# Optimization experiments

Hardware: AMD Instinct MI355X
Metric: run time of the kernel (lower is better)

Reference implementation:

```python
import jax, jax.numpy as jnp
import numpy as np

P, OBS, H, MSG, EMB, A = 2048, 512, 2048, 16, 32, 3
SLOPE = 0.01  # LeakyReLU default negative slope


def setup_inputs() -> dict:
    key = jax.random.key(0)
    ks = jax.random.split(key, 12)
    s = 0.02
    return {
        "obs": jax.random.normal(ks[0], (P, OBS), jnp.float32),
        "messages": jnp.zeros((P, MSG), jnp.float32),
        "embeddings": jnp.zeros((P, EMB), jnp.float32),
        "h": jnp.zeros((1, H), jnp.float32),
        "w_ih": jax.random.normal(ks[1], (3 * H, OBS), jnp.float32) * s,
        "w_hh": jax.random.normal(ks[2], (3 * H, H), jnp.float32) * s,
        "b_ih": jax.random.normal(ks[3], (3 * H,), jnp.float32) * s,
        "b_hh": jax.random.normal(ks[4], (3 * H,), jnp.float32) * s,
        "ff_w": jax.random.normal(ks[5], (2, H), jnp.float32) * s,
        "ff_b": jnp.zeros((2,), jnp.float32),
        "ap_w": jax.random.normal(ks[6], (A, H), jnp.float32) * s,
        "ap_b": jnp.zeros((A,), jnp.float32),
        "dp_w": jax.random.normal(ks[7], (A, H), jnp.float32) * s,
        "dp_b": jnp.zeros((A,), jnp.float32),
        "v_w": jax.random.normal(ks[8], (1, H), jnp.float32) * s,
        "v_b": jnp.zeros((1,), jnp.float32),
    }


def reference(obs, messages, embeddings, h, w_ih, w_hh, b_ih, b_hh,
              ff_w, ff_b, ap_w, ap_b, dp_w, dp_b, v_w, v_b):
    # h arg is ignored (module re-initializes it to zeros).
    hid = w_hh.shape[1]
    # precompute input-side GRU gates for all players: [P, 3H]
    gi_all = obs @ w_ih.T + b_ih

    def step(hc, gi):  # hc: [H]
        gh = hc @ w_hh.T + b_hh
        ir, iz, inn = jnp.split(gi, 3)
        hr, hz, hn = jnp.split(gh, 3)
        r = jax.nn.sigmoid(ir + hr)
        z = jax.nn.sigmoid(iz + hz)
        n = jnp.tanh(inn + r * hn)
        h_new = (1.0 - z) * n + z * hc
        return h_new, h_new

    h0 = jnp.zeros((hid,), obs.dtype)
    _, hs = jax.lax.scan(step, h0, gi_all)  # [P, H]

    acts = hs @ ff_w.T + ff_b                      # [P, 2]
    acts = jnp.where(acts >= 0, acts, SLOPE * acts)  # LeakyReLU
    a_w = jax.nn.softmax(acts[:, 0])               # softmax over players
    d_w = jax.nn.softmax(acts[:, 1])
    a_att = a_w @ hs                               # [H]
    d_att = d_w @ hs
    a_pol = a_att @ ap_w.T + ap_b
    d_pol = d_att @ dp_w.T + dp_b
    v = (a_att + d_att) @ v_w.T + v_b
    return (a_pol, d_pol, v)
```

## Files before the change

### kernel.cpp

```cpp
#include <hip/hip_runtime.h>
#include <cstdint>
#include <cstddef>

#define P_N  2048
#define OBS_N 512
#define H_N  2048
#define G3H  6144

__device__ __forceinline__ float wave_sum(float v) {
#pragma unroll
  for (int off = 32; off > 0; off >>= 1) v += __shfl_xor(v, off);
  return v;
}
__device__ __forceinline__ float wave_max(float v) {
#pragma unroll
  for (int off = 32; off > 0; off >>= 1) v = fmaxf(v, __shfl_xor(v, off));
  return v;
}

__global__ __launch_bounds__(256, 2) void gi_gemm(
    const float* __restrict__ A,
    const float* __restrict__ B,
    const float* __restrict__ bias,
    float* __restrict__ C)
{
  constexpr int BM = 128, BK = 32, LDP = BM + 4;
  __shared__ float As[BK][LDP];
  __shared__ float Bs[BK][LDP];
  const int tid = threadIdx.x;
  const int bm = blockIdx.y * BM;
  const int bn = blockIdx.x * BM;
  const int tx = tid & 15, ty = tid >> 4;
  const int lrow = tid >> 3;
  const int lk4  = (tid & 7) << 2;

  float acc[8][8];
#pragma unroll
  for (int i = 0; i < 8; ++i)
#pragma unroll
    for (int j = 0; j < 8; ++j) acc[i][j] = 0.f;

  for (int k0 = 0; k0 < OBS_N; k0 += BK) {
#pragma unroll
    for (int i = 0; i < 4; ++i) {
      const int r = lrow + 32 * i;
      float4 av = *(const float4*)(A + (size_t)(bm + r) * OBS_N + k0 + lk4);
      float4 bv = *(const float4*)(B + (size_t)(bn + r) * OBS_N + k0 + lk4);
      As[lk4 + 0][r] = av.x; As[lk4 + 1][r] = av.y;
      As[lk4 + 2][r] = av.z; As[lk4 + 3][r] = av.w;
      Bs[lk4 + 0][r] = bv.x; Bs[lk4 + 1][r] = bv.y;
      Bs[lk4 + 2][r] = bv.z; Bs[lk4 + 3][r] = bv.w;
    }
    __syncthreads();
#pragma unroll
    for (int k = 0; k < BK; ++k) {
      float4 a0 = *(const float4*)&As[k][ty * 4];
      float4 a1 = *(const float4*)&As[k][64 + ty * 4];
      float4 b0 = *(const float4*)&Bs[k][tx * 4];
      float4 b1 = *(const float4*)&Bs[k][64 + tx * 4];
      float a[8] = {a0.x, a0.y, a0.z, a0.w, a1.x, a1.y, a1.z, a1.w};
      float b[8] = {b0.x, b0.y, b0.z, b0.w, b1.x, b1.y, b1.z, b1.w};
#pragma unroll
      for (int i = 0; i < 8; ++i)
#pragma unroll
        for (int j = 0; j < 8; ++j)
          acc[i][j] = fmaf(a[i], b[j], acc[i][j]);
    }
    __syncthreads();
  }

  float4 bs0 = *(const float4*)(bias + bn + tx * 4);
  float4 bs1 = *(const float4*)(bias + bn + 64 + tx * 4);
  const float bb[8] = {bs0.x, bs0.y, bs0.z, bs0.w, bs1.x, bs1.y, bs1.z, bs1.w};
#pragma unroll
  for (int i = 0; i < 8; ++i) {
    const int row = bm + ((i < 4) ? (ty * 4 + i) : (64 + ty * 4 + i - 4));
    float4 o0 = {acc[i][0] + bb[0], acc[i][1] + bb[1], acc[i][2] + bb[2], acc[i][3] + bb[3]};
    float4 o1 = {acc[i][4] + bb[4], acc[i][5] + bb[5], acc[i][6] + bb[6], acc[i][7] + bb[7]};
    *(float4*)(C + (size_t)row * G3H + bn + tx * 4) = o0;
    *(float4*)(C + (size_t)row * G3H + bn + 64 + tx * 4) = o1;
  }
}

#define AGW(reg, val) \
  asm volatile("v_accvgpr_write_b32 " reg ", %0" :: "v"(val) : reg)
#define AGR(reg, dst) \
  asm volatile("v_accvgpr_read_b32 %0, " reg : "=v"(dst) :: reg)

#define LOADK_(koff, r0a,r0b,r0c,r0d, r1a,r1b,r1c,r1d, r2a,r2b,r2c,r2d) do { \
    float4 A_ = *(const float4*)(p0 + (koff) * 256 + l4); \
    float4 B_ = *(const float4*)(p1 + (koff) * 256 + l4); \
    float4 C_ = *(const float4*)(p2 + (koff) * 256 + l4); \
    AGW(r0a, A_.x); AGW(r0b, A_.y); AGW(r0c, A_.z); AGW(r0d, A_.w); \
    AGW(r1a, B_.x); AGW(r1b, B_.y); AGW(r1c, B_.z); AGW(r1d, B_.w); \
    AGW(r2a, C_.x); AGW(r2b, C_.y); AGW(r2c, C_.z); AGW(r2d, C_.w); \
  } while (0)

#define GEMVK_(koff, r0a,r0b,r0c,r0d, r1a,r1b,r1c,r1d, r2a,r2b,r2c,r2d) do { \
    float4 hv = *(const float4*)&hbuf[(koff) * 256 + l4]; \
    float tw; \
    AGR(r0a, tw); acc0 = fmaf(tw, hv.x, acc0); \
    AGR(r0b, tw); acc0 = fmaf(tw, hv.y, acc0); \
    AGR(r0c, tw); acc0 = fmaf(tw, hv.z, acc0); \
    AGR(r0d, tw); acc0 = fmaf(tw, hv.w, acc0); \
    AGR(r1a, tw); acc1 = fmaf(tw, hv.x, acc1); \
    AGR(r1b, tw); acc1 = fmaf(tw, hv.y, acc1); \
    AGR(r1c, tw); acc1 = fmaf(tw, hv.z, acc1); \
    AGR(r1d, tw); acc1 = fmaf(tw, hv.w, acc1); \
    AGR(r2a, tw); acc2 = fmaf(tw, hv.x, acc2); \
    AGR(r2b, tw); acc2 = fmaf(tw, hv.y, acc2); \
    AGR(r2c, tw); acc2 = fmaf(tw, hv.z, acc2); \
    AGR(r2d, tw); acc2 = fmaf(tw, hv.w, acc2); \
  } while (0)

#define LOADK(...) LOADK_(__VA_ARGS__)
#define GEMVK(...) GEMVK_(__VA_ARGS__)

#define KL0 "a0","a1","a2","a3",    "a32","a33","a34","a35", "a64","a65","a66","a67"
#define KL1 "a4","a5","a6","a7",    "a36","a37","a38","a39", "a68","a69","a70","a71"
#define KL2 "a8","a9","a10","a11",  "a40","a41","a42","a43", "a72","a73","a74","a75"
#define KL3 "a12","a13","a14","a15","a44","a45","a46","a47", "a76","a77","a78","a79"
#define KL4 "a16","a17","a18","a19","a48","a49","a50","a51", "a80","a81","a82","a83"
#define KL5 "a20","a21","a22","a23","a52","a53","a54","a55", "a84","a85","a86","a87"
#define KL6 "a24","a25","a26","a27","a56","a57","a58","a59", "a88","a89","a90","a91"
#define KL7 "a28","a29","a30","a31","a60","a61","a62","a63", "a92","a93","a94","a95"

__global__ __launch_bounds__(512, 1) void gru_scan(
    const float* __restrict__ w_hh,
    const float* __restrict__ b_hh,
    const float* __restrict__ gi,
    float* __restrict__ hs,
    unsigned long long* mb)
{
  __shared__ __align__(16) float hbuf[H_N];
  const int g   = blockIdx.x;
  const int tid = threadIdx.x;
  const int w   = tid >> 6;
  const int l   = tid & 63;
  const int l4  = l * 4;
  const int j   = (g << 3) + w;

  {
    const float* p0 = w_hh + (size_t)j * H_N;
    const float* p1 = w_hh + (size_t)(H_N + j) * H_N;
    const float* p2 = w_hh + (size_t)(2 * H_N + j) * H_N;
    LOADK(0, KL0); LOADK(1, KL1); LOADK(2, KL2); LOADK(3, KL3);
    LOADK(4, KL4); LOADK(5, KL5); LOADK(6, KL6); LOADK(7, KL7);
  }
  const float bh0 = b_hh[j], bh1 = b_hh[H_N + j], bh2 = b_hh[2 * H_N + j];
  float hprev = 0.f;

  for (int t = 0; t < P_N; ++t) {
    const float ir  = gi[(size_t)t * G3H + j];
    const float iz  = gi[(size_t)t * G3H + H_N + j];
    const float inn = gi[(size_t)t * G3H + 2 * H_N + j];

    float acc0 = 0.f, acc1 = 0.f, acc2 = 0.f;
    if (t > 0) {
      unsigned long long* src = mb + (size_t)((t - 1) & 1) * H_N + tid * 4;
      float h0 = 0.f, h1 = 0.f, h2 = 0.f, h3 = 0.f;
      unsigned pend = 0xFu;
      const unsigned tag = (unsigned)t;
      while (pend) {
#pragma unroll
        for (int q = 0; q < 4; ++q) {
          if (pend & (1u << q)) {
            unsigned long long v =
                __hip_atomic_load(src + q, __ATOMIC_RELAXED, __HIP_MEMORY_SCOPE_AGENT);
            if ((unsigned)(v >> 32) == tag) {
              float f = __uint_as_float((unsigned)(v & 0xffffffffull));
              if (q == 0) h0 = f; else if (q == 1) h1 = f;
              else if (q == 2) h2 = f; else h3 = f;
              pend &= ~(1u << q);
            }
          }
        }
        if (pend) __builtin_amdgcn_s_sleep(1);
      }
      __syncthreads();
      *(float4*)&hbuf[tid * 4] = make_float4(h0, h1, h2, h3);
      __syncthreads();

      GEMVK(0, KL0); GEMVK(1, KL1); GEMVK(2, KL2); GEMVK(3, KL3);
      GEMVK(4, KL4); GEMVK(5, KL5); GEMVK(6, KL6); GEMVK(7, KL7);

#pragma unroll
      for (int off = 32; off > 0; off >>= 1) {
        acc0 += __shfl_xor(acc0, off);
        acc1 += __shfl_xor(acc1, off);
        acc2 += __shfl_xor(acc2, off);
      }
    }

    const float r = 1.f / (1.f + __expf(-(ir + acc0 + bh0)));
    const float z = 1.f / (1.f + __expf(-(iz + acc1 + bh1)));
    const float narg = inn + r * (acc2 + bh2);
    const float e2 = __expf(2.f * narg);
    const float n = (e2 - 1.f) / (e2 + 1.f);
    const float hnew = (1.f - z) * n + z * hprev;
    hprev = hnew;

    if (l == 0) {
      hs[(size_t)t * H_N + j] = hnew;
      unsigned long long pk = ((unsigned long long)(unsigned)(t + 1) << 32) |
                              (unsigned long long)__float_as_uint(hnew);
      __hip_atomic_store(mb + (size_t)(t & 1) * H_N + j, pk,
                         __ATOMIC_RELAXED, __HIP_MEMORY_SCOPE_AGENT);
    }
  }
}

__global__ __launch_bounds__(512) void acts_kernel(
    const float* __restrict__ hs, const float* __restrict__ ff_w,
    const float* __restrict__ ff_b, float* __restrict__ acts)
{
  const int w = threadIdx.x >> 6, l = threadIdx.x & 63;
  const int p = blockIdx.x * 8 + w;
  const float* hrow = hs + (size_t)p * H_N;
  float sa = 0.f, sd = 0.f;
#pragma unroll
  for (int k = 0; k < 8; ++k) {
    float4 hv = *(const float4*)(hrow + k * 256 + l * 4);
    float4 fa = *(const float4*)(ff_w + k * 256 + l * 4);
    float4 fd = *(const float4*)(ff_w + H_N + k * 256 + l * 4);
    sa += hv.x * fa.x + hv.y * fa.y + hv.z * fa.z + hv.w * fa.w;
    sd += hv.x * fd.x + hv.y * fd.y + hv.z * fd.z + hv.w * fd.w;
  }
  sa = wave_sum(sa); sd = wave_sum(sd);
  if (l == 0) {
    float a = sa + ff_b[0];
    float d = sd + ff_b[1];
    a = (a >= 0.f) ? a : 0.01f * a;
    d = (d >= 0.f) ? d : 0.01f * d;
    acts[p] = a;
    acts[P_N + p] = d;
  }
}

__global__ __launch_bounds__(256) void softmax_kernel(
    const float* __restrict__ acts, float* __restrict__ wts)
{
  __shared__ float red[4];
  __shared__ float bcast;
  const int tid = threadIdx.x;
  const int w = tid >> 6, l = tid & 63;
  for (int c = 0; c < 2; ++c) {
    const float* x = acts + c * P_N;
    float* y = wts + c * P_N;
    float m = -3.4e38f;
    for (int i = tid; i < P_N; i += 256) m = fmaxf(m, x[i]);
    m = wave_max(m);
    if (l == 0) red[w] = m;
    __syncthreads();
    if (tid == 0) bcast = fmaxf(fmaxf(red[0], red[1]), fmaxf(red[2], red[3]));
    __syncthreads();
    const float M = bcast;
    float s = 0.f;
    for (int i = tid; i < P_N; i += 256) {
      float e = __expf(x[i] - M);
      y[i] = e;
      s += e;
    }
    s = wave_sum(s);
    __syncthreads();
    if (l == 0) red[w] = s;
    __syncthreads();
    if (tid == 0) bcast = 1.f / (red[0] + red[1] + red[2] + red[3]);
    __syncthreads();
    const float inv = bcast;
    for (int i = tid; i < P_N; i += 256) y[i] *= inv;
    __syncthreads();
  }
}

__global__ __launch_bounds__(256) void pool_kernel(
    const float* __restrict__ hs, const float* __restrict__ wts,
    float* __restrict__ att)
{
  const int g = blockIdx.x;
  const int tid = threadIdx.x;
  const int c0 = tid * 8;
  float aa[8] = {0, 0, 0, 0, 0, 0, 0, 0};
  float dd[8] = {0, 0, 0, 0, 0, 0, 0, 0};
  for (int r = 0; r < 16; ++r) {
    const int p = g * 16 + r;
    const float wa = wts[p];
    const float wd = wts[P_N + p];
    const float* hp = hs + (size_t)p * H_N + c0;
    float4 h0 = *(const float4*)hp;
    float4 h1 = *(const float4*)(hp + 4);
    aa[0] = fmaf(wa, h0.x, aa[0]); aa[1] = fmaf(wa, h0.y, aa[1]);
    aa[2] = fmaf(wa, h0.z, aa[2]); aa[3] = fmaf(wa, h0.w, aa[3]);
    aa[4] = fmaf(wa, h1.x, aa[4]); aa[5] = fmaf(wa, h1.y, aa[5]);
    aa[6] = fmaf(wa, h1.z, aa[6]); aa[7] = fmaf(wa, h1.w, aa[7]);
    dd[0] = fmaf(wd, h0.x, dd[0]); dd[1] = fmaf(wd, h0.y, dd[1]);
    dd[2] = fmaf(wd, h0.z, dd[2]); dd[3] = fmaf(wd, h0.w, dd[3]);
    dd[4] = fmaf(wd, h1.x, dd[4]); dd[5] = fmaf(wd, h1.y, dd[5]);
    dd[6] = fmaf(wd, h1.z, dd[6]); dd[7] = fmaf(wd, h1.w, dd[7]);
  }
#pragma unroll
  for (int q = 0; q < 8; ++q) {
    atomicAdd(&att[c0 + q], aa[q]);
    atomicAdd(&att[H_N + c0 + q], dd[q]);
  }
}

__global__ __launch_bounds__(512) void head_kernel(
    const float* __restrict__ att,
    const float* __restrict__ ap_w, const float* __restrict__ ap_b,
    const float* __restrict__ dp_w, const float* __restrict__ dp_b,
    const float* __restrict__ v_w, const float* __restrict__ v_b,
    float* __restrict__ out)
{
  const int w = threadIdx.x >> 6, l = threadIdx.x & 63;
  if (w >= 7) return;
  float s = 0.f;
  if (w < 3) {
    const float* m = ap_w + (size_t)w * H_N;
    for (int k = 0; k < 32; ++k) { int i = k * 64 + l; s += att[i] * m[i]; }
  } else if (w < 6) {
    const float* m = dp_w + (size_t)(w - 3) * H_N;
    for (int k = 0; k < 32; ++k) { int i = k * 64 + l; s += att[H_N + i] * m[i]; }
  } else {
    for (int k = 0; k < 32; ++k) { int i = k * 64 + l; s += (att[i] + att[H_N + i]) * v_w[i]; }
  }
  s = wave_sum(s);
  if (l == 0) {
    float b = (w < 3) ? ap_b[w] : ((w < 6) ? dp_b[w - 3] : v_b[0]);
    out[w] = s + b;
  }
}

extern "C" void kernel_launch(void* const* d_in, const int* in_sizes, int n_in,
                              void* d_out, int out_size, void* d_ws, size_t ws_size,
                              hipStream_t stream) {
  const float* obs  = (const float*)d_in[0];
  const float* w_ih = (const float*)d_in[4];
  const float* w_hh = (const float*)d_in[5];
  const float* b_ih = (const float*)d_in[6];
  const float* b_hh = (const float*)d_in[7];
  const float* ff_w = (const float*)d_in[8];
  const float* ff_b = (const float*)d_in[9];
  const float* ap_w = (const float*)d_in[10];
  const float* ap_b = (const float*)d_in[11];
  const float* dp_w = (const float*)d_in[12];
  const float* dp_b = (const float*)d_in[13];
  const float* v_w  = (const float*)d_in[14];
  const float* v_b  = (const float*)d_in[15];
  float* out = (float*)d_out;

  float* gi = (float*)d_ws;
  float* hs = gi + (size_t)P_N * G3H;
  unsigned long long* mb = (unsigned long long*)(hs + (size_t)P_N * H_N);
  float* acts = (float*)(mb + 2 * H_N);
  float* wts  = acts + 2 * P_N;
  float* att  = wts + 2 * P_N;

  hipMemsetAsync(mb, 0, 2 * H_N * sizeof(unsigned long long), stream);
  hipMemsetAsync(att, 0, 2 * H_N * sizeof(float), stream);

  gi_gemm<<<dim3(G3H / 128, P_N / 128), 256, 0, stream>>>(obs, w_ih, b_ih, gi);
  gru_scan<<<256, 512, 0, stream>>>(w_hh, b_hh, gi, hs, mb);
  acts_kernel<<<P_N / 8, 512, 0, stream>>>(hs, ff_w, ff_b, acts);
  softmax_kernel<<<1, 256, 0, stream>>>(acts, wts);
  pool_kernel<<<128, 256, 0, stream>>>(hs, wts, att);
  head_kernel<<<1, 512, 0, stream>>>(att, ap_w, ap_b, dp_w, dp_b, v_w, v_b, out);
}
```

Measured before the change: 10.89 ms.

## Add per-block step flags to GRU scan and write hs rows coalesced

Adds a per-block flag array that each workgroup bumps after finishing a step. Wave 0 polls all 256 flags before the other waves read the tagged hidden values, so most of the polling moves onto one wave. It also drops the scattered per-lane hs stores and has one rotating block write each full hs row from shared memory. The cost is an extra barrier and flag store per step, plus a second polling phase that may add latency on the critical path.

Measured after the change: 8.769 ms. 1.24x faster.

```diff
diff --git a/kernel.cpp b/kernel.cpp
--- a/kernel.cpp
+++ b/kernel.cpp
@@ -130,7 +130,8 @@
     const float* __restrict__ b_hh,
     const float* __restrict__ gi,
     float* __restrict__ hs,
-    unsigned long long* mb)
+    unsigned long long* mb,
+    unsigned* flags)
 {
   __shared__ __align__(16) float hbuf[H_N];
   const int g   = blockIdx.x;
@@ -157,10 +158,28 @@
 
     float acc0 = 0.f, acc1 = 0.f, acc2 = 0.f;
     if (t > 0) {
-      unsigned long long* src = mb + (size_t)((t - 1) & 1) * H_N + tid * 4;
+      const unsigned tag = (unsigned)t;
+      const int par = (t - 1) & 1;
+
+      if (w == 0) {
+        const unsigned long long exp2 =
+            (unsigned long long)tag * 0x100000001ULL;
+        unsigned long long* fp =
+            (unsigned long long*)(flags + (size_t)par * 256) + 2 * l;
+        for (;;) {
+          unsigned long long f0 =
+              __hip_atomic_load(fp + 0, __ATOMIC_RELAXED, __HIP_MEMORY_SCOPE_AGENT);
+          unsigned long long f1 =
+              __hip_atomic_load(fp + 1, __ATOMIC_RELAXED, __HIP_MEMORY_SCOPE_AGENT);
+          if (__all(f0 == exp2 && f1 == exp2)) break;
+          __builtin_amdgcn_s_sleep(1);
+        }
+      }
+      __syncthreads();
+
+      unsigned long long* src = mb + (size_t)par * H_N + tid * 4;
       float h0 = 0.f, h1 = 0.f, h2 = 0.f, h3 = 0.f;
       unsigned pend = 0xFu;
-      const unsigned tag = (unsigned)t;
       while (pend) {
 #pragma unroll
         for (int q = 0; q < 4; ++q) {
@@ -177,9 +196,13 @@
         }
         if (pend) __builtin_amdgcn_s_sleep(1);
       }
-      __syncthreads();
       *(float4*)&hbuf[tid * 4] = make_float4(h0, h1, h2, h3);
       __syncthreads();
+
+      if (g == ((t - 1) & 255)) {
+        *(float4*)(hs + (size_t)(t - 1) * H_N + tid * 4) =
+            *(const float4*)&hbuf[tid * 4];
+      }
 
       GEMVK(0, KL0); GEMVK(1, KL1); GEMVK(2, KL2); GEMVK(3, KL3);
       GEMVK(4, KL4); GEMVK(5, KL5); GEMVK(6, KL6); GEMVK(7, KL7);
@@ -201,13 +224,19 @@
     hprev = hnew;
 
     if (l == 0) {
-      hs[(size_t)t * H_N + j] = hnew;
       unsigned long long pk = ((unsigned long long)(unsigned)(t + 1) << 32) |
                               (unsigned long long)__float_as_uint(hnew);
       __hip_atomic_store(mb + (size_t)(t & 1) * H_N + j, pk,
                          __ATOMIC_RELAXED, __HIP_MEMORY_SCOPE_AGENT);
     }
-  }
+    __syncthreads();
+    if (tid == 0) {
+      __hip_atomic_store(flags + (size_t)(t & 1) * 256 + g, (unsigned)(t + 1),
+                         __ATOMIC_RELAXED, __HIP_MEMORY_SCOPE_AGENT);
+    }
+  }
+
+  if (l == 0) hs[(size_t)(P_N - 1) * H_N + j] = hprev;
 }
 
 __global__ __launch_bounds__(512) void acts_kernel(
@@ -352,15 +381,16 @@
   float* gi = (float*)d_ws;
   float* hs = gi + (size_t)P_N * G3H;
   unsigned long long* mb = (unsigned long long*)(hs + (size_t)P_N * H_N);
-  float* acts = (float*)(mb + 2 * H_N);
+  unsigned* flags = (unsigned*)(mb + 2 * H_N);
+  float* acts = (float*)(flags + 2 * 256);
   float* wts  = acts + 2 * P_N;
   float* att  = wts + 2 * P_N;
 
-  hipMemsetAsync(mb, 0, 2 * H_N * sizeof(unsigned long long), stream);
+  hipMemsetAsync(mb, 0, 2 * H_N * sizeof(unsigned long long) + 2 * 256 * sizeof(unsigned), stream);
   hipMemsetAsync(att, 0, 2 * H_N * sizeof(float), stream);
 
   gi_gemm<<<dim3(G3H / 128, P_N / 128), 256, 0, stream>>>(obs, w_ih, b_ih, gi);
-  gru_scan<<<256, 512, 0, stream>>>(w_hh, b_hh, gi, hs, mb);
+  gru_scan<<<256, 512, 0, stream>>>(w_hh, b_hh, gi, hs, mb, flags);
   acts_kernel<<<P_N / 8, 512, 0, stream>>>(hs, ff_w, ff_b, acts);
   softmax_kernel<<<1, 256, 0, stream>>>(acts, wts);
   pool_kernel<<<128, 256, 0, stream>>>(hs, wts, att);
```
